# Performance work log

Hardware: AMD Instinct MI355X
Metric: run time of the kernel (lower is better)

The kernel has to match this reference:

```python
import jax, jax.numpy as jnp
import numpy as np
from jax import lax

# Model dims (match init_kwargs)
B, CH, H, W = 32, 2, 32, 16
C_LEN, P_LEN, T_LEN = 3, 4, 4
POI_N, PT_F, T_FEAT, RP_N = 12, 9, 28, 4
OUTC = 8  # ResPlus out_channels
EPS = 1e-5


def conv1x1(x, w, b):
    # x: [B,C,H,W], w: [O,C,1,1] -> [B,O,H,W]
    return jnp.einsum('bchw,oc->bohw', x, w[:, :, 0, 0]) + b[None, :, None, None]


def conv3x3(x, w, b):
    y = lax.conv_general_dilated(x, w, (1, 1), 'SAME',
                                 dimension_numbers=('NCHW', 'OIHW', 'NCHW'))
    return y + b[None, :, None, None]


def bn(x, g, b, m, v):
    # eval-mode BatchNorm2d with running stats
    s = g / jnp.sqrt(v + EPS)
    return x * s[None, :, None, None] + (b - m * s)[None, :, None, None]


def forward(x, convc_w, convc_b, convp_w, convp_b, convt_w, convt_b,
            tm_w, tm_b, tf_w, tf_b, poi_w, poi_b,
            bn1_g, bn1_b, bn1_m, bn1_v, conv1_w, conv1_b,
            rp_bn1_g, rp_bn1_b, rp_bn1_m, rp_bn1_v, rp_conv1_w, rp_conv1_b,
            rp_bn2_g, rp_bn2_b, rp_bn2_m, rp_bn2_v, rp_conv2_w, rp_conv2_b,
            plus_w, plus_b, bn2_g, bn2_b, bn2_m, bn2_v, conv2_w, conv2_b):
    cut1 = CH * C_LEN
    cut2 = cut1 + CH * P_LEN
    cut3 = cut2 + CH * T_LEN
    c = conv1x1(x[:, :cut1], convc_w, convc_b)
    p = conv1x1(x[:, cut1:cut2], convp_w, convp_b)
    t = conv1x1(x[:, cut2:cut3], convt_w, convt_b)
    poi_in = x[:, -(POI_N + 31):-31]
    time_in = x[:, -31:]
    # PoI_trans / Time_trans
    tx = jax.nn.relu(conv1x1(time_in, tm_w, tm_b))
    tx = jax.nn.relu(conv1x1(tx, tf_w, tf_b))          # [B,1,H,W]
    poi_time = conv1x1(tx * poi_in, poi_w, poi_b)      # broadcast tile over PoI_N
    cpt = jnp.concatenate([c, p, t, poi_time], axis=1)
    cpt = bn(jax.nn.relu(cpt), bn1_g, bn1_b, bn1_m, bn1_v)
    cpt = conv1x1(cpt, conv1_w, conv1_b)               # [B,64,H,W]
    # ResPlus applied RP_N times with SHARED weights (self.net in a loop)
    plus_wf = plus_w.reshape(OUTC * H * W, -1)         # [8*H*W, 64*H*W]
    for _ in range(RP_N):
        z1 = conv3x3(jax.nn.relu(bn(cpt, rp_bn1_g, rp_bn1_b, rp_bn1_m, rp_bn1_v)),
                     rp_conv1_w, rp_conv1_b)           # [B,56,H,W]
        z2 = bn(jax.nn.relu(cpt), rp_bn1_g, rp_bn1_b, rp_bn1_m, rp_bn1_v)
        # plus_conv: full-map (H,W) kernel -> 1x1 spatial, i.e. a big GEMM
        z2 = (z2.reshape(B, -1) @ plus_wf.T + plus_b).reshape(B, OUTC, H, W)
        z3 = jax.nn.relu(bn(jnp.concatenate([z1, z2], axis=1),
                            rp_bn2_g, rp_bn2_b, rp_bn2_m, rp_bn2_v))
        cpt = conv3x3(z3, rp_conv2_w, rp_conv2_b) + cpt
    cpt2 = bn(jax.nn.relu(cpt), bn2_g, bn2_b, bn2_m, bn2_v)
    return jnp.tanh(conv1x1(cpt2, conv2_w, conv2_b))   # [B,2,H,W]


def setup_inputs() -> dict:
    key = jax.random.key(0)
    ks = iter(jax.random.split(key, 48))
    def rn(shape, s=0.05):
        return jax.random.normal(next(ks), shape, jnp.float32) * s
    def bnp(n):
        return (1.0 + rn((n,), 0.02), rn((n,)), rn((n,)),
                1.0 + 0.1 * jax.random.uniform(next(ks), (n,), jnp.float32))
    total_c = CH * (C_LEN + P_LEN + T_LEN) + POI_N + 31
    inp = {'x': jax.random.normal(next(ks), (B, total_c, H, W), jnp.float32)}
    inp['convc_w'], inp['convc_b'] = rn((64, CH * C_LEN, 1, 1)), rn((64,))
    inp['convp_w'], inp['convp_b'] = rn((64, CH * P_LEN, 1, 1)), rn((64,))
    inp['convt_w'], inp['convt_b'] = rn((64, CH * T_LEN, 1, 1)), rn((64,))
    inp['tm_w'], inp['tm_b'] = rn((T_FEAT, 31, 1, 1)), rn((T_FEAT,))
    inp['tf_w'], inp['tf_b'] = rn((1, T_FEAT, 1, 1)), rn((1,))
    inp['poi_w'], inp['poi_b'] = rn((PT_F, POI_N, 1, 1)), rn((PT_F,))
    inp['bn1_g'], inp['bn1_b'], inp['bn1_m'], inp['bn1_v'] = bnp(192 + PT_F)
    inp['conv1_w'], inp['conv1_b'] = rn((64, 192 + PT_F, 1, 1)), rn((64,))
    inp['rp_bn1_g'], inp['rp_bn1_b'], inp['rp_bn1_m'], inp['rp_bn1_v'] = bnp(64)
    inp['rp_conv1_w'], inp['rp_conv1_b'] = rn((64 - OUTC, 64, 3, 3)), rn((64 - OUTC,))
    inp['rp_bn2_g'], inp['rp_bn2_b'], inp['rp_bn2_m'], inp['rp_bn2_v'] = bnp(64)
    inp['rp_conv2_w'], inp['rp_conv2_b'] = rn((64, 64, 3, 3)), rn((64,))
    inp['plus_w'], inp['plus_b'] = rn((OUTC * H * W, 64, H, W), 0.01), rn((OUTC * H * W,))
    inp['bn2_g'], inp['bn2_b'], inp['bn2_m'], inp['bn2_v'] = bnp(64)
    inp['conv2_w'], inp['conv2_b'] = rn((2, 64, 1, 1)), rn((2,))
    return inp


def reference(x, convc_w, convc_b, convp_w, convp_b, convt_w, convt_b,
              tm_w, tm_b, tf_w, tf_b, poi_w, poi_b,
              bn1_g, bn1_b, bn1_m, bn1_v, conv1_w, conv1_b,
              rp_bn1_g, rp_bn1_b, rp_bn1_m, rp_bn1_v, rp_conv1_w, rp_conv1_b,
              rp_bn2_g, rp_bn2_b, rp_bn2_m, rp_bn2_v, rp_conv2_w, rp_conv2_b,
              plus_w, plus_b, bn2_g, bn2_b, bn2_m, bn2_v, conv2_w, conv2_b):
    return forward(x, convc_w, convc_b, convp_w, convp_b, convt_w, convt_b,
                   tm_w, tm_b, tf_w, tf_b, poi_w, poi_b,
                   bn1_g, bn1_b, bn1_m, bn1_v, conv1_w, conv1_b,
                   rp_bn1_g, rp_bn1_b, rp_bn1_m, rp_bn1_v, rp_conv1_w, rp_conv1_b,
                   rp_bn2_g, rp_bn2_b, rp_bn2_m, rp_bn2_v, rp_conv2_w, rp_conv2_b,
                   plus_w, plus_b, bn2_g, bn2_b, bn2_m, bn2_v, conv2_w, conv2_b)
```

## Files before the change

### kernel.cpp

```cpp
#include <hip/hip_runtime.h>
#include <cmath>

typedef __bf16 bf16x8 __attribute__((ext_vector_type(8)));
typedef float  f32x4  __attribute__((ext_vector_type(4)));
typedef float  f32x16 __attribute__((ext_vector_type(16)));

#define EPSF 1e-5f

__global__ __launch_bounds__(64) void head_kernel(
    const float* __restrict__ x,
    const float* __restrict__ cw, const float* __restrict__ cb,
    const float* __restrict__ pw, const float* __restrict__ pb,
    const float* __restrict__ tw, const float* __restrict__ tb,
    const float* __restrict__ tmw, const float* __restrict__ tmb,
    const float* __restrict__ tfw, const float* __restrict__ tfb,
    const float* __restrict__ poiw, const float* __restrict__ poib,
    const float* __restrict__ g1, const float* __restrict__ bb1,
    const float* __restrict__ m1, const float* __restrict__ v1,
    const float* __restrict__ w1, const float* __restrict__ b1c,
    float* __restrict__ cpt)
{
    int pix = blockIdx.x;
    int b = pix >> 9, p = pix & 511;
    int t = threadIdx.x;

    __shared__ float xs[65];
    __shared__ float tx1[28];
    __shared__ float y[201];
    __shared__ float tx2s;

    for (int c = t; c < 65; c += 64)
        xs[c] = x[(b * 65 + c) * 512 + p];
    __syncthreads();

    if (t < 28) {
        float acc = tmb[t];
        for (int j = 0; j < 31; ++j) acc += tmw[t * 31 + j] * xs[34 + j];
        tx1[t] = fmaxf(acc, 0.f);
    }
    __syncthreads();
    if (t == 0) {
        float acc = tfb[0];
        for (int j = 0; j < 28; ++j) acc += tfw[j] * tx1[j];
        tx2s = fmaxf(acc, 0.f);
    }
    __syncthreads();
    float tx2 = tx2s;

    {
        float acc = cb[t];
        for (int j = 0; j < 6; ++j) acc += cw[t * 6 + j] * xs[j];
        y[t] = acc;
    }
    {
        float acc = pb[t];
        for (int j = 0; j < 8; ++j) acc += pw[t * 8 + j] * xs[6 + j];
        y[64 + t] = acc;
    }
    {
        float acc = tb[t];
        for (int j = 0; j < 8; ++j) acc += tw[t * 8 + j] * xs[14 + j];
        y[128 + t] = acc;
    }
    if (t < 9) {
        float acc = poib[t];
        for (int j = 0; j < 12; ++j) acc += poiw[t * 12 + j] * (tx2 * xs[22 + j]);
        y[192 + t] = acc;
    }
    for (int c = t; c < 201; c += 64) {
        float s  = g1[c] * rsqrtf(v1[c] + EPSF);
        float tt = bb1[c] - m1[c] * s;
        y[c] = fmaxf(y[c], 0.f) * s + tt;
    }
    __syncthreads();

    float acc = b1c[t];
    const float* wrow = w1 + t * 201;
    for (int c = 0; c < 201; ++c) acc += wrow[c] * y[c];
    cpt[(b * 64 + t) * 512 + p] = acc;
}

__global__ void prep_kernel(const float* __restrict__ cpt,
                            const float* __restrict__ g, const float* __restrict__ bb,
                            const float* __restrict__ m, const float* __restrict__ v,
                            const float* __restrict__ plus_b,
                            __bf16* __restrict__ a_bf, float* __restrict__ z2)
{
    int i = blockIdx.x * blockDim.x + threadIdx.x;
    if (i < 32 * 64 * 512) {
        int c = (i >> 9) & 63;
        float s  = g[c] * rsqrtf(v[c] + EPSF);
        float tt = bb[c] - m[c] * s;
        a_bf[i] = (__bf16)(fmaxf(cpt[i], 0.f) * s + tt);
    }
    if (i < 32 * 4096) {
        z2[i] = plus_b[i & 4095];
    }
}

__global__ __launch_bounds__(256) void gemm_kernel(const __bf16* __restrict__ a_bf,
                                                   const float* __restrict__ plus_w,
                                                   float* __restrict__ z2)
{
    int wave = threadIdx.x >> 6;
    int lane = threadIdx.x & 63;
    int gw = blockIdx.x * 4 + wave;
    int nt = gw & 127;
    int ks = gw >> 7;
    int r32 = lane & 31;
    int hi  = lane >> 5;
    int n = nt * 32 + r32;
    long k0 = (long)ks * 2048 + hi * 8;

    const float*  wp = plus_w + (long)n * 32768 + k0;
    const bf16x8* ap = (const bf16x8*)(a_bf + (long)r32 * 32768 + k0);

    f32x16 acc = {};
#pragma unroll 4
    for (int it = 0; it < 128; ++it) {
        f32x4 w0 = *(const f32x4*)(wp + it * 16);
        f32x4 w1 = *(const f32x4*)(wp + it * 16 + 4);
        bf16x8 bfr;
#pragma unroll
        for (int j = 0; j < 4; ++j) { bfr[j] = (__bf16)w0[j]; bfr[j + 4] = (__bf16)w1[j]; }
        bf16x8 afr = ap[it * 2];
        acc = __builtin_amdgcn_mfma_f32_32x32x16_bf16(afr, bfr, acc, 0, 0, 0);
    }
#pragma unroll
    for (int r = 0; r < 16; ++r) {
        int brow = (r & 3) + 8 * (r >> 2) + 4 * hi;
        atomicAdd(&z2[brow * 4096 + n], acc[r]);
    }
}

__global__ __launch_bounds__(256) void gemm_convstore_kernel(const __bf16* __restrict__ a_bf,
                                                             const float* __restrict__ plus_w,
                                                             __bf16* __restrict__ w_bf,
                                                             float* __restrict__ z2)
{
    int wave = threadIdx.x >> 6;
    int lane = threadIdx.x & 63;
    int gw = blockIdx.x * 4 + wave;
    int nt = gw & 127;
    int ks = gw >> 7;
    int r32 = lane & 31;
    int hi  = lane >> 5;
    int n = nt * 32 + r32;
    long k0 = (long)ks * 2048 + hi * 8;

    const float*  wp  = plus_w + (long)n * 32768 + k0;
    __bf16*       wbp = w_bf   + (long)n * 32768 + k0;
    const bf16x8* ap  = (const bf16x8*)(a_bf + (long)r32 * 32768 + k0);

    f32x16 acc = {};
#pragma unroll 4
    for (int it = 0; it < 128; ++it) {
        f32x4 w0 = *(const f32x4*)(wp + it * 16);
        f32x4 w1 = *(const f32x4*)(wp + it * 16 + 4);
        bf16x8 bfr;
#pragma unroll
        for (int j = 0; j < 4; ++j) { bfr[j] = (__bf16)w0[j]; bfr[j + 4] = (__bf16)w1[j]; }
        *(bf16x8*)(wbp + it * 16) = bfr;
        bf16x8 afr = ap[it * 2];
        acc = __builtin_amdgcn_mfma_f32_32x32x16_bf16(afr, bfr, acc, 0, 0, 0);
    }
#pragma unroll
    for (int r = 0; r < 16; ++r) {
        int brow = (r & 3) + 8 * (r >> 2) + 4 * hi;
        atomicAdd(&z2[brow * 4096 + n], acc[r]);
    }
}

__global__ __launch_bounds__(256) void gemm_bf_kernel(const __bf16* __restrict__ a_bf,
                                                      const __bf16* __restrict__ w_bf,
                                                      float* __restrict__ z2)
{
    int wave = threadIdx.x >> 6;
    int lane = threadIdx.x & 63;
    int gw = blockIdx.x * 4 + wave;
    int nt = gw & 127;
    int ks = gw >> 7;
    int r32 = lane & 31;
    int hi  = lane >> 5;
    int n = nt * 32 + r32;
    long k0 = (long)ks * 2048 + hi * 8;

    const bf16x8* wpb = (const bf16x8*)(w_bf + (long)n * 32768 + k0);
    const bf16x8* ap  = (const bf16x8*)(a_bf + (long)r32 * 32768 + k0);

    f32x16 acc = {};
#pragma unroll 8
    for (int it = 0; it < 128; ++it) {
        acc = __builtin_amdgcn_mfma_f32_32x32x16_bf16(ap[it * 2], wpb[it * 2], acc, 0, 0, 0);
    }
#pragma unroll
    for (int r = 0; r < 16; ++r) {
        int brow = (r & 3) + 8 * (r >> 2) + 4 * hi;
        atomicAdd(&z2[brow * 4096 + n], acc[r]);
    }
}

__global__ __launch_bounds__(512) void conv1_kernel(const float* __restrict__ cpt,
                                                    const float* __restrict__ g, const float* __restrict__ bb,
                                                    const float* __restrict__ m, const float* __restrict__ v,
                                                    const float* __restrict__ w,
                                                    const float* __restrict__ bias,
                                                    float* __restrict__ z1)
{
    int b  = blockIdx.x;
    int og = blockIdx.y;
    int p  = threadIdx.x;
    int h = p >> 4, wc = p & 15;
    int o0 = og * 4;

    __shared__ float ss[64], ts[64];
    if (p < 64) {
        float s = g[p] * rsqrtf(v[p] + EPSF);
        ss[p] = s;
        ts[p] = bb[p] - m[p] * s;
    }
    __syncthreads();

    float a0 = bias[o0], a1 = bias[o0 + 1], a2 = bias[o0 + 2], a3 = bias[o0 + 3];
    const float* rb = cpt + b * 64 * 512;
    for (int c = 0; c < 64; ++c) {
        const float* rc = rb + c * 512;
        float s = ss[c], tt = ts[c];
        float rv[9];
#pragma unroll
        for (int dh = -1; dh <= 1; ++dh)
#pragma unroll
            for (int dw = -1; dw <= 1; ++dw) {
                int hh = h + dh, ww = wc + dw;
                bool ok = (hh >= 0) & (hh < 32) & (ww >= 0) & (ww < 16);
                rv[(dh + 1) * 3 + (dw + 1)] = ok ? fmaxf(rc[hh * 16 + ww] * s + tt, 0.f) : 0.f;
            }
#pragma unroll
        for (int tp = 0; tp < 9; ++tp) {
            a0 += rv[tp] * w[((o0    ) * 64 + c) * 9 + tp];
            a1 += rv[tp] * w[((o0 + 1) * 64 + c) * 9 + tp];
            a2 += rv[tp] * w[((o0 + 2) * 64 + c) * 9 + tp];
            a3 += rv[tp] * w[((o0 + 3) * 64 + c) * 9 + tp];
        }
    }
    float* zb = z1 + ((b * 56 + o0) * 512) + p;
    zb[0] = a0; zb[512] = a1; zb[1024] = a2; zb[1536] = a3;
}

__global__ void prep2_kernel(const float* __restrict__ z1, const float* __restrict__ z2,
                             const float* __restrict__ g, const float* __restrict__ bb,
                             const float* __restrict__ m, const float* __restrict__ v,
                             __bf16* __restrict__ z3)
{
    int i = blockIdx.x * blockDim.x + threadIdx.x;
    if (i >= 32 * 64 * 512) return;
    int b = i >> 15, c = (i >> 9) & 63, p = i & 511;
    float val = (c < 56) ? z1[(b * 56 + c) * 512 + p]
                         : z2[b * 4096 + (c - 56) * 512 + p];
    float s  = g[c] * rsqrtf(v[c] + EPSF);
    float tt = bb[c] - m[c] * s;
    z3[i] = (__bf16)fmaxf(val * s + tt, 0.f);
}

__global__ __launch_bounds__(512) void conv2_kernel(const __bf16* __restrict__ z3,
                                                    const float* __restrict__ w,
                                                    const float* __restrict__ bias,
                                                    float* __restrict__ cpt)
{
    int b  = blockIdx.x;
    int og = blockIdx.y;
    int p  = threadIdx.x;
    int h = p >> 4, wc = p & 15;
    int o0 = og * 4;
    float a0 = bias[o0], a1 = bias[o0 + 1], a2 = bias[o0 + 2], a3 = bias[o0 + 3];
    const __bf16* rb = z3 + b * 64 * 512;
    for (int c = 0; c < 64; ++c) {
        const __bf16* rc = rb + c * 512;
        float rv[9];
#pragma unroll
        for (int dh = -1; dh <= 1; ++dh)
#pragma unroll
            for (int dw = -1; dw <= 1; ++dw) {
                int hh = h + dh, ww = wc + dw;
                bool ok = (hh >= 0) & (hh < 32) & (ww >= 0) & (ww < 16);
                rv[(dh + 1) * 3 + (dw + 1)] = ok ? (float)rc[hh * 16 + ww] : 0.f;
            }
#pragma unroll
        for (int tp = 0; tp < 9; ++tp) {
            a0 += rv[tp] * w[((o0    ) * 64 + c) * 9 + tp];
            a1 += rv[tp] * w[((o0 + 1) * 64 + c) * 9 + tp];
            a2 += rv[tp] * w[((o0 + 2) * 64 + c) * 9 + tp];
            a3 += rv[tp] * w[((o0 + 3) * 64 + c) * 9 + tp];
        }
    }
    float* cb_ = cpt + ((b * 64 + o0) * 512) + p;
    cb_[0]    += a0;
    cb_[512]  += a1;
    cb_[1024] += a2;
    cb_[1536] += a3;
}

__global__ void tail_kernel(const float* __restrict__ cpt,
                            const float* __restrict__ g, const float* __restrict__ bb,
                            const float* __restrict__ m, const float* __restrict__ v,
                            const float* __restrict__ w2, const float* __restrict__ b2,
                            float* __restrict__ out)
{
    int i = blockIdx.x * blockDim.x + threadIdx.x;
    if (i >= 32 * 512) return;
    int b = i >> 9, p = i & 511;
    float a0 = b2[0], a1 = b2[1];
    for (int c = 0; c < 64; ++c) {
        float s  = g[c] * rsqrtf(v[c] + EPSF);
        float tt = bb[c] - m[c] * s;
        float y = fmaxf(cpt[(b * 64 + c) * 512 + p], 0.f) * s + tt;
        a0 += w2[c] * y;
        a1 += w2[64 + c] * y;
    }
    out[(b * 2 + 0) * 512 + p] = tanhf(a0);
    out[(b * 2 + 1) * 512 + p] = tanhf(a1);
}

extern "C" void kernel_launch(void* const* d_in, const int* in_sizes, int n_in,
                              void* d_out, int out_size, void* d_ws, size_t ws_size,
                              hipStream_t stream)
{
#define IN(i) ((const float*)d_in[i])
    float*  cpt  = (float*)d_ws;
    __bf16* a_bf = (__bf16*)((char*)d_ws + (size_t)4 * 1024 * 1024);
    __bf16* z3   = a_bf;
    float*  z1   = (float*)((char*)d_ws + (size_t)6 * 1024 * 1024);
    float*  z2   = z1 + 32 * 56 * 512;
    __bf16* w_bf = (__bf16*)((char*)d_ws + (size_t)10 * 1024 * 1024);

    const bool cacheW = ws_size >= (size_t)266 * 1024 * 1024;

    head_kernel<<<16384, 64, 0, stream>>>(
        IN(0), IN(1), IN(2), IN(3), IN(4), IN(5), IN(6), IN(7), IN(8), IN(9), IN(10),
        IN(11), IN(12), IN(13), IN(14), IN(15), IN(16), IN(17), IN(18), cpt);

    for (int it = 0; it < 4; ++it) {
        prep_kernel<<<4096, 256, 0, stream>>>(cpt, IN(19), IN(20), IN(21), IN(22),
                                              IN(32), a_bf, z2);
        if (cacheW) {
            if (it == 0)
                gemm_convstore_kernel<<<512, 256, 0, stream>>>(a_bf, IN(31), w_bf, z2);
            else
                gemm_bf_kernel<<<512, 256, 0, stream>>>(a_bf, w_bf, z2);
        } else {
            gemm_kernel<<<512, 256, 0, stream>>>(a_bf, IN(31), z2);
        }
        conv1_kernel<<<dim3(32, 14), 512, 0, stream>>>(cpt, IN(19), IN(20), IN(21), IN(22),
                                                       IN(23), IN(24), z1);
        prep2_kernel<<<4096, 256, 0, stream>>>(z1, z2, IN(25), IN(26), IN(27), IN(28), z3);
        conv2_kernel<<<dim3(32, 16), 512, 0, stream>>>(z3, IN(29), IN(30), cpt);
    }

    tail_kernel<<<64, 256, 0, stream>>>(cpt, IN(33), IN(34), IN(35), IN(36),
                                        IN(37), IN(38), (float*)d_out);
#undef IN
}
```

Measured before the change: 1.880 ms.

## Prefetch GEMM operands via global_load_lds ring and convert weights in separate kernel

Result: faster. 1.832 ms (-2.5%).

```diff
diff --git a/kernel.cpp b/kernel.cpp
--- a/kernel.cpp
+++ b/kernel.cpp
@@ -1,11 +1,22 @@
 #include <hip/hip_runtime.h>
 #include <cmath>
+#include <cstdint>
 
 typedef __bf16 bf16x8 __attribute__((ext_vector_type(8)));
 typedef float  f32x4  __attribute__((ext_vector_type(4)));
 typedef float  f32x16 __attribute__((ext_vector_type(16)));
 
 #define EPSF 1e-5f
+
+__device__ __forceinline__ void gll16(const void* g, void* l)
+{
+    __builtin_amdgcn_global_load_lds(
+        reinterpret_cast<const __attribute__((address_space(1))) void*>(
+            reinterpret_cast<uintptr_t>(g)),
+        reinterpret_cast<__attribute__((address_space(3))) void*>(
+            reinterpret_cast<uintptr_t>(l)),
+        16, 0, 0);
+}
 
 __global__ __launch_bounds__(64) void head_kernel(
     const float* __restrict__ x,
@@ -80,6 +91,18 @@
     cpt[(b * 64 + t) * 512 + p] = acc;
 }
 
+__global__ __launch_bounds__(256) void wconv_kernel(const float* __restrict__ w,
+                                                    __bf16* __restrict__ wb)
+{
+    long i = ((long)blockIdx.x * 256 + threadIdx.x) * 8;
+    f32x4 a = *(const f32x4*)(w + i);
+    f32x4 b = *(const f32x4*)(w + i + 4);
+    bf16x8 o;
+#pragma unroll
+    for (int j = 0; j < 4; ++j) { o[j] = (__bf16)a[j]; o[j + 4] = (__bf16)b[j]; }
+    *(bf16x8*)(wb + i) = o;
+}
+
 __global__ void prep_kernel(const float* __restrict__ cpt,
                             const float* __restrict__ g, const float* __restrict__ bb,
                             const float* __restrict__ m, const float* __restrict__ v,
@@ -133,11 +156,12 @@
     }
 }
 
-__global__ __launch_bounds__(256) void gemm_convstore_kernel(const __bf16* __restrict__ a_bf,
-                                                             const float* __restrict__ plus_w,
-                                                             __bf16* __restrict__ w_bf,
-                                                             float* __restrict__ z2)
-{
+__global__ __launch_bounds__(256) void gemm_lds_kernel(const __bf16* __restrict__ a_bf,
+                                                       const __bf16* __restrict__ w_bf,
+                                                       float* __restrict__ z2)
+{
+    __shared__ __bf16 ring[4][2][8][512];
+
     int wave = threadIdx.x >> 6;
     int lane = threadIdx.x & 63;
     int gw = blockIdx.x * 4 + wave;
@@ -148,51 +172,38 @@
     int n = nt * 32 + r32;
     long k0 = (long)ks * 2048 + hi * 8;
 
-    const float*  wp  = plus_w + (long)n * 32768 + k0;
-    __bf16*       wbp = w_bf   + (long)n * 32768 + k0;
-    const bf16x8* ap  = (const bf16x8*)(a_bf + (long)r32 * 32768 + k0);
+    const __bf16* wsrc = w_bf + (long)n   * 32768 + k0;
+    const __bf16* asrc = a_bf + (long)r32 * 32768 + k0;
+    __bf16* wr = &ring[wave][0][0][0];
+    __bf16* ar = &ring[wave][1][0][0];
+
+#pragma unroll
+    for (int s = 0; s < 8; ++s) {
+        gll16(wsrc + s * 16, wr + s * 512);
+        gll16(asrc + s * 16, ar + s * 512);
+    }
 
     f32x16 acc = {};
-#pragma unroll 4
-    for (int it = 0; it < 128; ++it) {
-        f32x4 w0 = *(const f32x4*)(wp + it * 16);
-        f32x4 w1 = *(const f32x4*)(wp + it * 16 + 4);
-        bf16x8 bfr;
-#pragma unroll
-        for (int j = 0; j < 4; ++j) { bfr[j] = (__bf16)w0[j]; bfr[j + 4] = (__bf16)w1[j]; }
-        *(bf16x8*)(wbp + it * 16) = bfr;
-        bf16x8 afr = ap[it * 2];
+    for (int it = 0; it < 120; ++it) {
+        int slot = it & 7;
+        asm volatile("s_waitcnt vmcnt(14)" ::: "memory");
+        __builtin_amdgcn_sched_barrier(0);
+        bf16x8 bfr = *(const bf16x8*)(wr + slot * 512 + lane * 8);
+        bf16x8 afr = *(const bf16x8*)(ar + slot * 512 + lane * 8);
         acc = __builtin_amdgcn_mfma_f32_32x32x16_bf16(afr, bfr, acc, 0, 0, 0);
-    }
-#pragma unroll
-    for (int r = 0; r < 16; ++r) {
-        int brow = (r & 3) + 8 * (r >> 2) + 4 * hi;
-        atomicAdd(&z2[brow * 4096 + n], acc[r]);
-    }
-}
-
-__global__ __launch_bounds__(256) void gemm_bf_kernel(const __bf16* __restrict__ a_bf,
-                                                      const __bf16* __restrict__ w_bf,
-                                                      float* __restrict__ z2)
-{
-    int wave = threadIdx.x >> 6;
-    int lane = threadIdx.x & 63;
-    int gw = blockIdx.x * 4 + wave;
-    int nt = gw & 127;
-    int ks = gw >> 7;
-    int r32 = lane & 31;
-    int hi  = lane >> 5;
-    int n = nt * 32 + r32;
-    long k0 = (long)ks * 2048 + hi * 8;
-
-    const bf16x8* wpb = (const bf16x8*)(w_bf + (long)n * 32768 + k0);
-    const bf16x8* ap  = (const bf16x8*)(a_bf + (long)r32 * 32768 + k0);
-
-    f32x16 acc = {};
-#pragma unroll 8
-    for (int it = 0; it < 128; ++it) {
-        acc = __builtin_amdgcn_mfma_f32_32x32x16_bf16(ap[it * 2], wpb[it * 2], acc, 0, 0, 0);
-    }
+        gll16(wsrc + (it + 8) * 16, wr + slot * 512);
+        gll16(asrc + (it + 8) * 16, ar + slot * 512);
+    }
+    asm volatile("s_waitcnt vmcnt(0)" ::: "memory");
+    __builtin_amdgcn_sched_barrier(0);
+#pragma unroll
+    for (int it = 120; it < 128; ++it) {
+        int slot = it & 7;
+        bf16x8 bfr = *(const bf16x8*)(wr + slot * 512 + lane * 8);
+        bf16x8 afr = *(const bf16x8*)(ar + slot * 512 + lane * 8);
+        acc = __builtin_amdgcn_mfma_f32_32x32x16_bf16(afr, bfr, acc, 0, 0, 0);
+    }
+
 #pragma unroll
     for (int r = 0; r < 16; ++r) {
         int brow = (r & 3) + 8 * (r >> 2) + 4 * hi;
@@ -335,6 +346,9 @@
 
     const bool cacheW = ws_size >= (size_t)266 * 1024 * 1024;
 
+    if (cacheW)
+        wconv_kernel<<<65536, 256, 0, stream>>>(IN(31), w_bf);
+
     head_kernel<<<16384, 64, 0, stream>>>(
         IN(0), IN(1), IN(2), IN(3), IN(4), IN(5), IN(6), IN(7), IN(8), IN(9), IN(10),
         IN(11), IN(12), IN(13), IN(14), IN(15), IN(16), IN(17), IN(18), cpt);
@@ -342,14 +356,10 @@
     for (int it = 0; it < 4; ++it) {
         prep_kernel<<<4096, 256, 0, stream>>>(cpt, IN(19), IN(20), IN(21), IN(22),
                                               IN(32), a_bf, z2);
-        if (cacheW) {
-            if (it == 0)
-                gemm_convstore_kernel<<<512, 256, 0, stream>>>(a_bf, IN(31), w_bf, z2);
-            else
-                gemm_bf_kernel<<<512, 256, 0, stream>>>(a_bf, w_bf, z2);
-        } else {
+        if (cacheW)
+            gemm_lds_kernel<<<512, 256, 0, stream>>>(a_bf, w_bf, z2);
+        else
             gemm_kernel<<<512, 256, 0, stream>>>(a_bf, IN(31), z2);
-        }
         conv1_kernel<<<dim3(32, 14), 512, 0, stream>>>(cpt, IN(19), IN(20), IN(21), IN(22),
                                                        IN(23), IN(24), z1);
         prep2_kernel<<<4096, 256, 0, stream>>>(z1, z2, IN(25), IN(26), IN(27), IN(28), z3);
```
